# Performance work log

Measured on AMD Instinct MI355X. Metric: run time of the kernel, lower is better.

Reference implementation:

```python
import jax, jax.numpy as jnp
import numpy as np

HIDDEN = 1024
D_INNER = 2048      # expand * hidden
STATE = 16          # state_dim n
DT_RANK = 64        # ceil(hidden/16)
D_CONV = 4
B, S = 2, 2048
EPS = 1e-5


def setup_inputs() -> dict:
    key = jax.random.key(0)
    ks = jax.random.split(key, 10)
    sc = lambda fan_in: 1.0 / np.sqrt(fan_in)
    x = jax.random.normal(ks[0], (B, S, HIDDEN), dtype=jnp.float32)
    norm_w = jnp.ones((HIDDEN,), dtype=jnp.float32)
    in_proj_w = jax.random.uniform(ks[1], (2 * D_INNER, HIDDEN), minval=-sc(HIDDEN), maxval=sc(HIDDEN), dtype=jnp.float32)
    conv_w = jax.random.uniform(ks[2], (D_INNER, 1, D_CONV), minval=-sc(D_CONV), maxval=sc(D_CONV), dtype=jnp.float32)
    conv_b = jax.random.uniform(ks[3], (D_INNER,), minval=-sc(D_CONV), maxval=sc(D_CONV), dtype=jnp.float32)
    x_proj_w = jax.random.uniform(ks[4], (DT_RANK + 2 * STATE, D_INNER), minval=-sc(D_INNER), maxval=sc(D_INNER), dtype=jnp.float32)
    dt_proj_w = jax.random.uniform(ks[5], (D_INNER, DT_RANK), minval=-sc(DT_RANK), maxval=sc(DT_RANK), dtype=jnp.float32)
    dt_proj_b = jax.random.uniform(ks[6], (D_INNER,), minval=-sc(DT_RANK), maxval=sc(DT_RANK), dtype=jnp.float32)
    A_log = jnp.log(jnp.broadcast_to(jnp.arange(1, STATE + 1, dtype=jnp.float32), (D_INNER, STATE)))
    D = jnp.ones((D_INNER,), dtype=jnp.float32)
    out_proj_w = jax.random.uniform(ks[7], (HIDDEN, D_INNER), minval=-sc(D_INNER), maxval=sc(D_INNER), dtype=jnp.float32)
    return {"x": x, "norm_w": norm_w, "in_proj_w": in_proj_w, "conv_w": conv_w,
            "conv_b": conv_b, "x_proj_w": x_proj_w, "dt_proj_w": dt_proj_w,
            "dt_proj_b": dt_proj_b, "A_log": A_log, "D": D, "out_proj_w": out_proj_w}


def _selective_scan(u, delta, A, Bm, Cm, D):
    # u, delta: [b,s,d]; A: [d,n]; Bm, Cm: [b,s,n]; D: [d]
    deltaA = jnp.exp(jnp.einsum('bsd,dn->bsdn', delta, A))          # [b,s,d,n]
    deltaB_u = jnp.einsum('bsd,bsn,bsd->bsdn', delta, Bm, u)        # [b,s,d,n]

    def step(h, inp):
        dA_t, dBu_t, C_t = inp                                       # [b,d,n],[b,d,n],[b,n]
        h = dA_t * h + dBu_t
        y = jnp.einsum('bdn,bn->bd', h, C_t)
        return h, y

    h0 = jnp.zeros((u.shape[0], u.shape[2], A.shape[1]), dtype=u.dtype)
    _, ys = jax.lax.scan(step, h0,
                         (deltaA.transpose(1, 0, 2, 3),
                          deltaB_u.transpose(1, 0, 2, 3),
                          Cm.transpose(1, 0, 2)))
    y = ys.transpose(1, 0, 2)                                        # [b,s,d]
    return y + u * D


def reference(x, norm_w, in_proj_w, conv_w, conv_b, x_proj_w, dt_proj_w,
              dt_proj_b, A_log, D, out_proj_w):
    # RMSNorm
    xn = x * jax.lax.rsqrt(jnp.mean(x * x, axis=-1, keepdims=True) + EPS) * norm_w

    # in_proj -> split
    x_and_res = xn @ in_proj_w.T                                     # [b,s,2*d_inner]
    xi, res = jnp.split(x_and_res, 2, axis=-1)

    # causal depthwise conv1d (left-pad d_conv-1, truncate to s)
    xc = jax.lax.conv_general_dilated(
        xi.transpose(0, 2, 1), conv_w,
        window_strides=(1,), padding=[(D_CONV - 1, 0)],
        dimension_numbers=('NCH', 'OIH', 'NCH'),
        feature_group_count=D_INNER) + conv_b[None, :, None]
    xc = jax.nn.silu(xc.transpose(0, 2, 1))                          # [b,s,d_inner]

    # ssm
    A = -jnp.exp(A_log)
    x_dbl = xc @ x_proj_w.T                                          # [b,s,dt_rank+2n]
    dt, Bm, Cm = jnp.split(x_dbl, [DT_RANK, DT_RANK + STATE], axis=-1)
    delta = jax.nn.softplus(dt @ dt_proj_w.T + dt_proj_b)            # [b,s,d_inner]
    y = _selective_scan(xc, delta, A, Bm, Cm, D)

    y = y * jax.nn.silu(res)
    out = y @ out_proj_w.T
    return out + x
```

## Files before the change

kernel.cpp:

```cpp
#include <hip/hip_runtime.h>
#include <math.h>

#define HIDDEN   1024
#define D_INNER  2048
#define NSTATE   16
#define DT_RANK  64
#define BATCH    2
#define SEQ      2048
#define T_TOK    (BATCH * SEQ)
#define XDBL     (DT_RANK + 2 * NSTATE)
#define NCH      64
#define CHL      (SEQ / NCH)
#define BDN      (BATCH * D_INNER * NSTATE)

typedef float f32x4   __attribute__((ext_vector_type(4)));
typedef short bf16x8  __attribute__((ext_vector_type(8)));
typedef short short4v __attribute__((ext_vector_type(4)));

#define AS1 __attribute__((address_space(1)))
#define AS3 __attribute__((address_space(3)))
#define GLOAD(src, dst) __builtin_amdgcn_global_load_lds( \
    (const AS1 unsigned int*)(src), (AS3 unsigned int*)(dst), 16, 0, 0)

__device__ __forceinline__ float silu_f(float x) { return x / (1.0f + __expf(-x)); }
__device__ __forceinline__ float softplus_f(float x) {
    return fmaxf(x, 0.0f) + log1pf(__expf(-fabsf(x)));
}
__device__ __forceinline__ unsigned short f2bf(float x) {
    unsigned int u = __float_as_uint(x);
    u += 0x7fffu + ((u >> 16) & 1u);
    return (unsigned short)(u >> 16);
}
__device__ __forceinline__ float bf2f(unsigned short h) {
    return __uint_as_float(((unsigned int)h) << 16);
}

template<int SEGS>
__global__ __launch_bounds__(256) void wpack_kernel(
        const float* __restrict__ w, unsigned short* __restrict__ wp, int K) {
    int i = blockIdx.x * 256 + threadIdx.x;
    int kq = K >> 2;
    int row = i / kq;
    int c = (i - row * kq) << 2;
    float4 v = *(const float4*)(w + (size_t)row * K + c);
    short4v hi, lo;
    hi.x = f2bf(v.x); hi.y = f2bf(v.y); hi.z = f2bf(v.z); hi.w = f2bf(v.w);
    lo.x = f2bf(v.x - bf2f(hi.x)); lo.y = f2bf(v.y - bf2f(hi.y));
    lo.z = f2bf(v.z - bf2f(hi.z)); lo.w = f2bf(v.w - bf2f(hi.w));
    size_t b0 = (size_t)row * (SEGS * K) + c;
    *(short4v*)(wp + b0) = hi;
    if (SEGS == 2) *(short4v*)(wp + b0 + K) = lo;
}

__global__ __launch_bounds__(256) void rmsnorm_pack_kernel(
        const float* __restrict__ x, const float* __restrict__ w,
        unsigned short* __restrict__ xn_p) {
    int row = blockIdx.x;
    float4 v = ((const float4*)(x + (size_t)row * HIDDEN))[threadIdx.x];
    float ss = v.x*v.x + v.y*v.y + v.z*v.z + v.w*v.w;
    #pragma unroll
    for (int off = 32; off; off >>= 1) ss += __shfl_down(ss, off);
    __shared__ float wsum[4];
    if ((threadIdx.x & 63) == 0) wsum[threadIdx.x >> 6] = ss;
    __syncthreads();
    float scale = rsqrtf((wsum[0] + wsum[1] + wsum[2] + wsum[3]) / (float)HIDDEN + 1e-5f);
    float4 wv = ((const float4*)w)[threadIdx.x];
    float o0 = v.x * scale * wv.x, o1 = v.y * scale * wv.y;
    float o2 = v.z * scale * wv.z, o3 = v.w * scale * wv.w;
    short4v hi, lo;
    hi.x = f2bf(o0); hi.y = f2bf(o1); hi.z = f2bf(o2); hi.w = f2bf(o3);
    lo.x = f2bf(o0 - bf2f(hi.x)); lo.y = f2bf(o1 - bf2f(hi.y));
    lo.z = f2bf(o2 - bf2f(hi.z)); lo.w = f2bf(o3 - bf2f(hi.w));
    size_t b0 = (size_t)row * (2 * HIDDEN) + threadIdx.x * 4;
    *(short4v*)&xn_p[b0]          = hi;
    *(short4v*)&xn_p[b0 + HIDDEN] = lo;
}

__global__ __launch_bounds__(256, 2) void mgemm_in_kernel(
        const unsigned short* __restrict__ Ap,
        const unsigned short* __restrict__ Wp,
        float* __restrict__ C0, float* __restrict__ C1) {
    __shared__ short Ah[128 * 64];
    __shared__ short Al[128 * 64];
    __shared__ short Bh[256 * 64];
    const int t = threadIdx.x;
    const int w = t >> 6, l = t & 63;
    const int m0 = blockIdx.y * 128, n0 = blockIdx.x * 256;
    const int lrow = l & 15;
    f32x4 acc[8][4];
    #pragma unroll
    for (int m = 0; m < 8; ++m)
        #pragma unroll
        for (int n = 0; n < 4; ++n) {
            acc[m][n].x = 0.f; acc[m][n].y = 0.f; acc[m][n].z = 0.f; acc[m][n].w = 0.f;
        }
    const int srow8 = l >> 3;
    const int sc8   = (l & 7) ^ srow8;
    const unsigned short* ga = Ap + (size_t)(m0 + w * 32 + srow8) * 2048 + sc8 * 8;
    const unsigned short* gb = Wp + (size_t)(n0 + w * 64 + srow8) * 1024 + sc8 * 8;
    for (int k0 = 0; k0 < 1024; k0 += 64) {
        __syncthreads();
        #pragma unroll
        for (int q = 0; q < 4; ++q) {
            const int ar = (w * 32 + q * 8) * 128;
            GLOAD(ga + k0 + (size_t)q * 8 * 2048,        (char*)Ah + ar);
            GLOAD(ga + 1024 + k0 + (size_t)q * 8 * 2048, (char*)Al + ar);
        }
        #pragma unroll
        for (int q = 0; q < 8; ++q)
            GLOAD(gb + k0 + (size_t)q * 8 * 1024, (char*)Bh + (w * 64 + q * 8) * 128);
        __syncthreads();
        #pragma unroll
        for (int kk = 0; kk < 2; ++kk) {
            const int slot = ((kk * 4 + (l >> 4)) ^ (l & 7)) * 8;
            bf16x8 bh[4];
            #pragma unroll
            for (int n = 0; n < 4; ++n)
                bh[n] = *(const bf16x8*)&Bh[(w * 64 + n * 16 + lrow) * 64 + slot];
            #pragma unroll
            for (int m = 0; m < 8; ++m) {
                bf16x8 ah = *(const bf16x8*)&Ah[(m * 16 + lrow) * 64 + slot];
                bf16x8 al = *(const bf16x8*)&Al[(m * 16 + lrow) * 64 + slot];
                #pragma unroll
                for (int n = 0; n < 4; ++n) {
                    acc[m][n] = __builtin_amdgcn_mfma_f32_16x16x32_bf16(
                        ah, bh[n], acc[m][n], 0, 0, 0);
                    acc[m][n] = __builtin_amdgcn_mfma_f32_16x16x32_bf16(
                        al, bh[n], acc[m][n], 0, 0, 0);
                }
            }
        }
    }
    float* dst = (n0 < D_INNER) ? C0 : C1;
    const int cbase = (n0 < D_INNER) ? n0 : n0 - D_INNER;
    #pragma unroll
    for (int m = 0; m < 8; ++m) {
        #pragma unroll
        for (int n = 0; n < 4; ++n) {
            #pragma unroll
            for (int j = 0; j < 4; ++j) {
                int row = m0 + m * 16 + (l >> 4) * 4 + j;
                int col = cbase + w * 64 + n * 16 + (l & 15);
                dst[(size_t)row * D_INNER + col] = acc[m][n][j];
            }
        }
    }
}

template<int TERMS, int EPI>
__global__ __launch_bounds__(256) void mgemm_kernel(
        const unsigned short* __restrict__ Ap, const unsigned short* __restrict__ Wp,
        int Klog, int klen, int brows, float* __restrict__ C0, float* __restrict__ C1,
        int splitN, int ldout, size_t partStride, const float* __restrict__ bias) {
    constexpr int NT = (TERMS == 3) ? 4 : 3;
    __shared__ short lds[NT * 128 * 64];
    short* Ah = lds;
    short* Al = lds + 128 * 64;
    short* Bh = lds + 2 * 128 * 64;
    short* Bl = lds + 3 * 128 * 64;
    const int t = threadIdx.x;
    const int w = t >> 6, l = t & 63;
    const int m0 = blockIdx.y * 128, n0 = blockIdx.x * 128;
    const int kbeg = blockIdx.z * klen;
    const int wr = (w >> 1) * 64, wc = (w & 1) * 64;
    const int lrow = l & 15;
    f32x4 acc[4][4];
    #pragma unroll
    for (int m = 0; m < 4; ++m)
        #pragma unroll
        for (int n = 0; n < 4; ++n) {
            acc[m][n].x = 0.f; acc[m][n].y = 0.f; acc[m][n].z = 0.f; acc[m][n].w = 0.f;
        }
    const int Asr = 2 * Klog;
    const int Wsr = (TERMS == 3) ? 2 * Klog : Klog;
    const int srow = w * 32 + (l >> 3);
    const int sc8  = (l & 7) ^ ((l >> 3) & 7);
    const int brow = min(n0 + srow, brows - 1);
    const unsigned short* ga = Ap + (size_t)(m0 + srow) * Asr + sc8 * 8;
    const unsigned short* gb = Wp + (size_t)brow * Wsr + sc8 * 8;
    for (int k0 = kbeg; k0 < kbeg + klen; k0 += 64) {
        __syncthreads();
        #pragma unroll
        for (int q = 0; q < 4; ++q) {
            const int doff = (w * 32 + q * 8) * 128;
            GLOAD(ga + k0 + (size_t)q * 8 * Asr,        (char*)Ah + doff);
            GLOAD(ga + Klog + k0 + (size_t)q * 8 * Asr, (char*)Al + doff);
            GLOAD(gb + k0 + (size_t)q * 8 * Wsr,        (char*)Bh + doff);
            if (TERMS == 3)
                GLOAD(gb + Klog + k0 + (size_t)q * 8 * Wsr, (char*)Bl + doff);
        }
        __syncthreads();
        #pragma unroll
        for (int kk = 0; kk < 2; ++kk) {
            const int slot = ((kk * 4 + (l >> 4)) ^ (l & 7)) * 8;
            bf16x8 ah[4], al[4], bh[4], bl[4];
            #pragma unroll
            for (int m = 0; m < 4; ++m) {
                ah[m] = *(const bf16x8*)&Ah[(wr + m * 16 + lrow) * 64 + slot];
                al[m] = *(const bf16x8*)&Al[(wr + m * 16 + lrow) * 64 + slot];
            }
            #pragma unroll
            for (int n = 0; n < 4; ++n) {
                bh[n] = *(const bf16x8*)&Bh[(wc + n * 16 + lrow) * 64 + slot];
                if (TERMS == 3)
                    bl[n] = *(const bf16x8*)&Bl[(wc + n * 16 + lrow) * 64 + slot];
            }
            #pragma unroll
            for (int m = 0; m < 4; ++m)
                #pragma unroll
                for (int n = 0; n < 4; ++n) {
                    acc[m][n] = __builtin_amdgcn_mfma_f32_16x16x32_bf16(
                        ah[m], bh[n], acc[m][n], 0, 0, 0);
                    acc[m][n] = __builtin_amdgcn_mfma_f32_16x16x32_bf16(
                        al[m], bh[n], acc[m][n], 0, 0, 0);
                    if (TERMS == 3)
                        acc[m][n] = __builtin_amdgcn_mfma_f32_16x16x32_bf16(
                            ah[m], bl[n], acc[m][n], 0, 0, 0);
                }
        }
    }
    float* dst = (EPI == 2) ? (C0 + blockIdx.z * partStride) : C0;
    #pragma unroll
    for (int m = 0; m < 4; ++m) {
        #pragma unroll
        for (int n = 0; n < 4; ++n) {
            #pragma unroll
            for (int j = 0; j < 4; ++j) {
                int row = m0 + wr + m * 16 + (l >> 4) * 4 + j;
                int col = n0 + wc + n * 16 + (l & 15);
                float v = acc[m][n][j];
                if (EPI == 2) {
                    dst[(size_t)row * ldout + col] = v;
                } else {
                    C0[(size_t)row * ldout + col] = softplus_f(v + bias[col]);
                }
            }
        }
    }
}

__global__ __launch_bounds__(256) void reduce2_kernel(
        const float* __restrict__ parts, size_t partStride,
        const float* __restrict__ x, float* __restrict__ out) {
    size_t i = (size_t)blockIdx.x * 256 + threadIdx.x;
    float4 a = ((const float4*)(parts))[i];
    float4 b = ((const float4*)(parts + partStride))[i];
    float4 xv = ((const float4*)x)[i];
    float4 o;
    o.x = a.x + b.x + xv.x;
    o.y = a.y + b.y + xv.y;
    o.z = a.z + b.z + xv.z;
    o.w = a.w + b.w + xv.w;
    ((float4*)out)[i] = o;
}

__global__ __launch_bounds__(256) void reduceX_kernel(
        const float* __restrict__ parts, float* __restrict__ xdbl,
        unsigned short* __restrict__ dtp) {
    int i = blockIdx.x * 256 + threadIdx.x;
    int row = i / 24;
    int c = (i - row * 24) * 4;
    float4 s = make_float4(0.f, 0.f, 0.f, 0.f);
    #pragma unroll
    for (int z = 0; z < 8; ++z) {
        float4 a = *(const float4*)(parts + (size_t)z * 524288 + (size_t)row * 128 + c);
        s.x += a.x; s.y += a.y; s.z += a.z; s.w += a.w;
    }
    *(float4*)(xdbl + (size_t)row * XDBL + c) = s;
    if (c < DT_RANK) {
        short4v hi, lo;
        hi.x = f2bf(s.x); hi.y = f2bf(s.y); hi.z = f2bf(s.z); hi.w = f2bf(s.w);
        lo.x = f2bf(s.x - bf2f(hi.x)); lo.y = f2bf(s.y - bf2f(hi.y));
        lo.z = f2bf(s.z - bf2f(hi.z)); lo.w = f2bf(s.w - bf2f(hi.w));
        size_t b0 = (size_t)row * 128 + c;
        *(short4v*)(dtp + b0)      = hi;
        *(short4v*)(dtp + b0 + 64) = lo;
    }
}

__global__ __launch_bounds__(256) void conv_silu_kernel(
        const float* __restrict__ xi, const float* __restrict__ w,
        const float* __restrict__ b, unsigned short* __restrict__ xc_p) {
    size_t i = (size_t)blockIdx.x * 256 + threadIdx.x;
    int d = (int)(i & (D_INNER - 1));
    int tt = (int)(i >> 11);
    int s = tt & (SEQ - 1);
    float4 wv = ((const float4*)w)[d];
    float acc = b[d];
    if (s >= 3) acc += wv.x * xi[i - 3 * D_INNER];
    if (s >= 2) acc += wv.y * xi[i - 2 * D_INNER];
    if (s >= 1) acc += wv.z * xi[i - 1 * D_INNER];
    acc += wv.w * xi[i];
    float o = silu_f(acc);
    unsigned short hi = f2bf(o);
    unsigned short lo = f2bf(o - bf2f(hi));
    size_t o2 = (size_t)tt * (2 * D_INNER) + d;
    xc_p[o2]           = hi;
    xc_p[o2 + D_INNER] = lo;
}


__global__ __launch_bounds__(256) void scanA_kernel(
        const unsigned short* __restrict__ xcp, const float* __restrict__ delta,
        const float* __restrict__ xdbl, const float* __restrict__ A_log,
        float* __restrict__ hpart, float* __restrict__ Pp) {
    const int bid = blockIdx.x;
    const int b    = bid >> 9;
    const int c    = (bid >> 3) & 63;
    const int dblk = bid & 7;
    const int d    = (dblk << 8) + threadIdx.x;
    float adn[NSTATE];
    #pragma unroll
    for (int k = 0; k < 4; ++k) {
        float4 a = *(const float4*)(A_log + d * NSTATE + k * 4);
        adn[k*4+0] = -__expf(a.x); adn[k*4+1] = -__expf(a.y);
        adn[k*4+2] = -__expf(a.z); adn[k*4+3] = -__expf(a.w);
    }
    float h[NSTATE], P[NSTATE];
    #pragma unroll
    for (int n = 0; n < NSTATE; ++n) { h[n] = 0.f; P[n] = 1.f; }
    const int rowbase = b * SEQ + c * CHL;
    #pragma unroll 4
    for (int r = 0; r < CHL; ++r) {
        const int row = rowbase + r;
        const float* brow = xdbl + (size_t)row * XDBL + DT_RANK;
        size_t o2 = (size_t)row * (2 * D_INNER) + d;
        float dl = delta[(size_t)row * D_INNER + d];
        float u  = bf2f(xcp[o2]) + bf2f(xcp[o2 + D_INNER]);
        float du = dl * u;
        #pragma unroll
        for (int n = 0; n < NSTATE; ++n) {
            float dA = __expf(dl * adn[n]);
            h[n] = fmaf(dA, h[n], du * brow[n]);
            P[n] *= dA;
        }
    }
    size_t base = (size_t)c * BDN + (size_t)(b * D_INNER + d) * NSTATE;
    #pragma unroll
    for (int k = 0; k < 4; ++k) {
        *(float4*)(hpart + base + k * 4) = make_float4(h[k*4], h[k*4+1], h[k*4+2], h[k*4+3]);
        *(float4*)(Pp    + base + k * 4) = make_float4(P[k*4], P[k*4+1], P[k*4+2], P[k*4+3]);
    }
}

__global__ __launch_bounds__(256) void scanB_kernel(
        const float* __restrict__ hpart, const float* __restrict__ Pp,
        float* __restrict__ hstart) {
    int idx = blockIdx.x * 256 + threadIdx.x;
    float h = 0.f;
    for (int c = 0; c < NCH; ++c) {
        hstart[(size_t)c * BDN + idx] = h;
        h = fmaf(Pp[(size_t)c * BDN + idx], h, hpart[(size_t)c * BDN + idx]);
    }
}

__global__ __launch_bounds__(256) void scanC_kernel(
        const unsigned short* xcp, const float* __restrict__ delta,
        const float* __restrict__ xdbl, const float* __restrict__ A_log,
        const float* __restrict__ Dp, const float* __restrict__ hstart,
        const float* __restrict__ res, unsigned short* y_p) {
    const int bid = blockIdx.x;
    const int b    = bid >> 9;
    const int c    = (bid >> 3) & 63;
    const int dblk = bid & 7;
    const int d    = (dblk << 8) + threadIdx.x;
    float adn[NSTATE];
    #pragma unroll
    for (int k = 0; k < 4; ++k) {
        float4 a = *(const float4*)(A_log + d * NSTATE + k * 4);
        adn[k*4+0] = -__expf(a.x); adn[k*4+1] = -__expf(a.y);
        adn[k*4+2] = -__expf(a.z); adn[k*4+3] = -__expf(a.w);
    }
    const float Dd = Dp[d];
    float h[NSTATE];
    size_t base = (size_t)c * BDN + (size_t)(b * D_INNER + d) * NSTATE;
    #pragma unroll
    for (int k = 0; k < 4; ++k) {
        float4 hv = *(const float4*)(hstart + base + k * 4);
        h[k*4] = hv.x; h[k*4+1] = hv.y; h[k*4+2] = hv.z; h[k*4+3] = hv.w;
    }
    const int rowbase = b * SEQ + c * CHL;
    #pragma unroll 4
    for (int r = 0; r < CHL; ++r) {
        const int row = rowbase + r;
        const float* brow = xdbl + (size_t)row * XDBL + DT_RANK;
        const float* crow = brow + NSTATE;
        size_t o2 = (size_t)row * (2 * D_INNER) + d;
        float dl = delta[(size_t)row * D_INNER + d];
        float u  = bf2f(xcp[o2]) + bf2f(xcp[o2 + D_INNER]);
        float du = dl * u;
        float ys[4];
        ys[0] = u * Dd; ys[1] = 0.f; ys[2] = 0.f; ys[3] = 0.f;
        #pragma unroll
        for (int n = 0; n < NSTATE; ++n) {
            float dA = __expf(dl * adn[n]);
            h[n] = fmaf(dA, h[n], du * brow[n]);
            ys[n & 3] = fmaf(h[n], crow[n], ys[n & 3]);
        }
        float ysum = (ys[0] + ys[1]) + (ys[2] + ys[3]);
        float rv = res[(size_t)row * D_INNER + d];
        float gv = ysum * silu_f(rv);
        unsigned short hi = f2bf(gv);
        unsigned short lo = f2bf(gv - bf2f(hi));
        y_p[o2]           = hi;
        y_p[o2 + D_INNER] = lo;
    }
}

extern "C" void kernel_launch(void* const* d_in, const int* in_sizes, int n_in,
                              void* d_out, int out_size, void* d_ws, size_t ws_size,
                              hipStream_t stream) {
    const float* x         = (const float*)d_in[0];
    const float* norm_w    = (const float*)d_in[1];
    const float* in_proj_w = (const float*)d_in[2];
    const float* conv_w    = (const float*)d_in[3];
    const float* conv_b    = (const float*)d_in[4];
    const float* x_proj_w  = (const float*)d_in[5];
    const float* dt_proj_w = (const float*)d_in[6];
    const float* dt_proj_b = (const float*)d_in[7];
    const float* A_log     = (const float*)d_in[8];
    const float* Dp        = (const float*)d_in[9];
    const float* out_proj_w= (const float*)d_in[10];
    float* out = (float*)d_out;
    float* ws  = (float*)d_ws;

    const size_t M8 = (size_t)T_TOK * D_INNER;
    float* res   = ws;
    float* delta = res + M8;
    float* xdbl  = delta + M8;
    unsigned short* xn_p   = (unsigned short*)(xdbl + (size_t)T_TOK * XDBL);
    unsigned short* w_in_p = xn_p   + (size_t)4096 * 2048;
    unsigned short* w_out_p= w_in_p + (size_t)4096 * 1024;
    unsigned short* w_xp_p = w_out_p+ (size_t)1024 * 4096;
    unsigned short* w_dt_p = w_xp_p + (size_t)96 * 4096;
    unsigned short* xc_p   = w_dt_p + (size_t)2048 * 128;
    unsigned short* dtp_p  = xc_p   + (size_t)4096 * 4096;
    float* xi    = (float*)(dtp_p + (size_t)4096 * 128);
    float* hpart = xi;
    float* Pp    = xi + (size_t)BDN * NCH;
    float* hstart= (float*)xn_p;
    float* parts_x = delta;
    unsigned short* y_p = xc_p;
    float* parts = ws;
    const size_t partStride = (size_t)T_TOK * HIDDEN;

    wpack_kernel<1><<<4096, 256, 0, stream>>>(in_proj_w,  w_in_p,  HIDDEN);
    wpack_kernel<2><<<2048, 256, 0, stream>>>(out_proj_w, w_out_p, D_INNER);
    wpack_kernel<2><<<192,  256, 0, stream>>>(x_proj_w,   w_xp_p,  D_INNER);
    wpack_kernel<2><<<128,  256, 0, stream>>>(dt_proj_w,  w_dt_p,  DT_RANK);

    rmsnorm_pack_kernel<<<T_TOK, 256, 0, stream>>>(x, norm_w, xn_p);

    {
        dim3 g(4096 / 256, T_TOK / 128, 1);
        mgemm_in_kernel<<<g, 256, 0, stream>>>(xn_p, w_in_p, xi, res);
    }

    conv_silu_kernel<<<(int)(M8 / 256), 256, 0, stream>>>(xi, conv_w, conv_b, xc_p);

    {
        dim3 g(1, T_TOK / 128, 8);
        mgemm_kernel<3, 2><<<g, 256, 0, stream>>>(xc_p, w_xp_p, D_INNER, D_INNER / 8,
                                                  96, parts_x, nullptr, 0, 128, 524288, nullptr);
    }
    reduceX_kernel<<<T_TOK * 24 / 256, 256, 0, stream>>>(parts_x, xdbl, dtp_p);

    {
        dim3 g(D_INNER / 128, T_TOK / 128, 1);
        mgemm_kernel<3, 3><<<g, 256, 0, stream>>>(dtp_p, w_dt_p, DT_RANK, DT_RANK,
                                                  D_INNER, delta, nullptr, 0, D_INNER, 0, dt_proj_b);
    }

    scanA_kernel<<<BATCH * NCH * 8, 256, 0, stream>>>(xc_p, delta, xdbl, A_log, hpart, Pp);
    scanB_kernel<<<BDN / 256, 256, 0, stream>>>(hpart, Pp, hstart);
    scanC_kernel<<<BATCH * NCH * 8, 256, 0, stream>>>(xc_p, delta, xdbl, A_log, Dp, hstart, res, y_p);

    {
        dim3 g(HIDDEN / 128, T_TOK / 128, 2);
        mgemm_kernel<3, 2><<<g, 256, 0, stream>>>(y_p, w_out_p, D_INNER, D_INNER / 2,
                                                  HIDDEN, parts, nullptr, 0, HIDDEN, partStride, nullptr);
    }
    reduce2_kernel<<<(int)(partStride / 4 / 256), 256, 0, stream>>>(parts, partStride, x, out);
}
```

Before: 312.7 us.

## Add 8-wave double-buffered 256x256 split-bf16 GEMM for in/out projections

Replaces the in_proj GEMM and the out_proj GEMM with a new 512-thread kernel using a 256x256 tile. It double-buffers LDS stages and interleaves global-to-LDS loads with MFMA phases, using barriers and s_setprio. Operands are packed as concatenated hi/lo (and hi/hi/lo) K segments, so each term pair runs as a single longer K loop. The out projection uses a 4-way K split with a 4-way reduce, and the workspace layout is rearranged. This adds barrier overhead and more packed data in exchange for better MFMA utilisation and load overlap.

```diff
diff --git a/kernel.cpp b/kernel.cpp
--- a/kernel.cpp
+++ b/kernel.cpp
@@ -35,7 +35,7 @@
     return __uint_as_float(((unsigned int)h) << 16);
 }
 
-template<int SEGS>
+template<int MODE>
 __global__ __launch_bounds__(256) void wpack_kernel(
         const float* __restrict__ w, unsigned short* __restrict__ wp, int K) {
     int i = blockIdx.x * 256 + threadIdx.x;
@@ -47,9 +47,18 @@
     hi.x = f2bf(v.x); hi.y = f2bf(v.y); hi.z = f2bf(v.z); hi.w = f2bf(v.w);
     lo.x = f2bf(v.x - bf2f(hi.x)); lo.y = f2bf(v.y - bf2f(hi.y));
     lo.z = f2bf(v.z - bf2f(hi.z)); lo.w = f2bf(v.w - bf2f(hi.w));
-    size_t b0 = (size_t)row * (SEGS * K) + c;
-    *(short4v*)(wp + b0) = hi;
-    if (SEGS == 2) *(short4v*)(wp + b0 + K) = lo;
+    size_t b0 = (size_t)row * ((MODE == 2 ? 3 : 2) * K) + c;
+    if (MODE == 0) {
+        *(short4v*)(wp + b0)     = hi;
+        *(short4v*)(wp + b0 + K) = lo;
+    } else if (MODE == 1) {
+        *(short4v*)(wp + b0)     = hi;
+        *(short4v*)(wp + b0 + K) = hi;
+    } else {
+        *(short4v*)(wp + b0)         = hi;
+        *(short4v*)(wp + b0 + K)     = lo;
+        *(short4v*)(wp + b0 + 2 * K) = hi;
+    }
 }
 
 __global__ __launch_bounds__(256) void rmsnorm_pack_kernel(
@@ -76,17 +85,21 @@
     *(short4v*)&xn_p[b0 + HIDDEN] = lo;
 }
 
-__global__ __launch_bounds__(256, 2) void mgemm_in_kernel(
-        const unsigned short* __restrict__ Ap,
-        const unsigned short* __restrict__ Wp,
-        float* __restrict__ C0, float* __restrict__ C1) {
-    __shared__ short Ah[128 * 64];
-    __shared__ short Al[128 * 64];
-    __shared__ short Bh[256 * 64];
+template<int EPI>
+__global__ __launch_bounds__(512, 2) void mgemm8_kernel(
+        const unsigned short* __restrict__ Ap, const unsigned short* __restrict__ Wp,
+        int Kp, int klen, float* __restrict__ C0, float* __restrict__ C1,
+        int ldout, size_t partStride) {
+    __shared__ short lds8[65536];
     const int t = threadIdx.x;
     const int w = t >> 6, l = t & 63;
-    const int m0 = blockIdx.y * 128, n0 = blockIdx.x * 256;
+    const int wm = w >> 2, wn = w & 3;
+    const int m0 = blockIdx.y * 256, n0 = blockIdx.x * 256;
+    const int kbeg = blockIdx.z * klen;
+    const int NT = klen >> 6;
     const int lrow = l & 15;
+    const int sl0 = (((l >> 4)    ) ^ (l & 7)) * 8;
+    const int sl1 = (((l >> 4) + 4) ^ (l & 7)) * 8;
     f32x4 acc[8][4];
     #pragma unroll
     for (int m = 0; m < 8; ++m)
@@ -96,52 +109,112 @@
         }
     const int srow8 = l >> 3;
     const int sc8   = (l & 7) ^ srow8;
-    const unsigned short* ga = Ap + (size_t)(m0 + w * 32 + srow8) * 2048 + sc8 * 8;
-    const unsigned short* gb = Wp + (size_t)(n0 + w * 64 + srow8) * 1024 + sc8 * 8;
-    for (int k0 = 0; k0 < 1024; k0 += 64) {
-        __syncthreads();
-        #pragma unroll
-        for (int q = 0; q < 4; ++q) {
-            const int ar = (w * 32 + q * 8) * 128;
-            GLOAD(ga + k0 + (size_t)q * 8 * 2048,        (char*)Ah + ar);
-            GLOAD(ga + 1024 + k0 + (size_t)q * 8 * 2048, (char*)Al + ar);
-        }
-        #pragma unroll
-        for (int q = 0; q < 8; ++q)
-            GLOAD(gb + k0 + (size_t)q * 8 * 1024, (char*)Bh + (w * 64 + q * 8) * 128);
-        __syncthreads();
-        #pragma unroll
-        for (int kk = 0; kk < 2; ++kk) {
-            const int slot = ((kk * 4 + (l >> 4)) ^ (l & 7)) * 8;
-            bf16x8 bh[4];
+    const unsigned short* gA = Ap + (size_t)(m0 + w * 8 + srow8) * Kp + kbeg + sc8 * 8;
+    const unsigned short* gB = Wp + (size_t)(n0 + w * 8 + srow8) * Kp + kbeg + sc8 * 8;
+    auto stageA = [&](int c, int koff) {
+        #pragma unroll
+        for (int hq = 0; hq < 4; ++hq)
+            GLOAD(gA + (size_t)(hq * 64) * Kp + koff,
+                  (char*)lds8 + ((c * 2 + (hq >> 1)) * 16384)
+                              + ((hq & 1) * 64 + w * 8) * 128);
+    };
+    auto stageB = [&](int c, int koff) {
+        #pragma unroll
+        for (int hq = 0; hq < 4; ++hq)
+            GLOAD(gB + (size_t)(hq * 64) * Kp + koff,
+                  (char*)lds8 + 65536 + ((c * 2 + (hq >> 1)) * 16384)
+                              + ((hq & 1) * 64 + w * 8) * 128);
+    };
+    stageA(0, 0);
+    stageB(0, 0);
+    asm volatile("s_waitcnt vmcnt(0)" ::: "memory");
+    __builtin_amdgcn_s_barrier();
+    for (int tt = 0; tt < NT; ++tt) {
+        const int c = tt & 1;
+        const int knext = (tt + 1) * 64;
+        const bool more = (tt + 1 < NT);
+        const short* Ab = lds8 + (c * 2 + wm) * 8192;
+        const short* Bb = lds8 + 32768 + (c * 2 + (wn >> 1)) * 8192;
+        const int br0 = (wn & 1) * 64;
+        bf16x8 bh[4], af[4];
+        #pragma unroll
+        for (int n = 0; n < 4; ++n)
+            bh[n] = *(const bf16x8*)&Bb[(br0 + n * 16 + lrow) * 64 + sl0];
+        #pragma unroll
+        for (int m = 0; m < 4; ++m)
+            af[m] = *(const bf16x8*)&Ab[(m * 16 + lrow) * 64 + sl0];
+        if (more) stageA(c ^ 1, knext);
+        __builtin_amdgcn_s_barrier();
+        asm volatile("s_waitcnt lgkmcnt(0)" ::: "memory");
+        __builtin_amdgcn_s_setprio(1);
+        #pragma unroll
+        for (int m = 0; m < 4; ++m)
             #pragma unroll
             for (int n = 0; n < 4; ++n)
-                bh[n] = *(const bf16x8*)&Bh[(w * 64 + n * 16 + lrow) * 64 + slot];
-            #pragma unroll
-            for (int m = 0; m < 8; ++m) {
-                bf16x8 ah = *(const bf16x8*)&Ah[(m * 16 + lrow) * 64 + slot];
-                bf16x8 al = *(const bf16x8*)&Al[(m * 16 + lrow) * 64 + slot];
-                #pragma unroll
-                for (int n = 0; n < 4; ++n) {
-                    acc[m][n] = __builtin_amdgcn_mfma_f32_16x16x32_bf16(
-                        ah, bh[n], acc[m][n], 0, 0, 0);
-                    acc[m][n] = __builtin_amdgcn_mfma_f32_16x16x32_bf16(
-                        al, bh[n], acc[m][n], 0, 0, 0);
-                }
-            }
-        }
-    }
-    float* dst = (n0 < D_INNER) ? C0 : C1;
-    const int cbase = (n0 < D_INNER) ? n0 : n0 - D_INNER;
+                acc[m][n] = __builtin_amdgcn_mfma_f32_16x16x32_bf16(
+                    af[m], bh[n], acc[m][n], 0, 0, 0);
+        __builtin_amdgcn_s_setprio(0);
+        __builtin_amdgcn_s_barrier();
+        #pragma unroll
+        for (int m = 0; m < 4; ++m)
+            af[m] = *(const bf16x8*)&Ab[((m + 4) * 16 + lrow) * 64 + sl0];
+        if (more) stageB(c ^ 1, knext);
+        __builtin_amdgcn_s_barrier();
+        asm volatile("s_waitcnt lgkmcnt(0)" ::: "memory");
+        __builtin_amdgcn_s_setprio(1);
+        #pragma unroll
+        for (int m = 0; m < 4; ++m)
+            #pragma unroll
+            for (int n = 0; n < 4; ++n)
+                acc[m + 4][n] = __builtin_amdgcn_mfma_f32_16x16x32_bf16(
+                    af[m], bh[n], acc[m + 4][n], 0, 0, 0);
+        __builtin_amdgcn_s_setprio(0);
+        __builtin_amdgcn_s_barrier();
+        #pragma unroll
+        for (int n = 0; n < 4; ++n)
+            bh[n] = *(const bf16x8*)&Bb[(br0 + n * 16 + lrow) * 64 + sl1];
+        #pragma unroll
+        for (int m = 0; m < 4; ++m)
+            af[m] = *(const bf16x8*)&Ab[(m * 16 + lrow) * 64 + sl1];
+        __builtin_amdgcn_s_barrier();
+        asm volatile("s_waitcnt lgkmcnt(0)" ::: "memory");
+        __builtin_amdgcn_s_setprio(1);
+        #pragma unroll
+        for (int m = 0; m < 4; ++m)
+            #pragma unroll
+            for (int n = 0; n < 4; ++n)
+                acc[m][n] = __builtin_amdgcn_mfma_f32_16x16x32_bf16(
+                    af[m], bh[n], acc[m][n], 0, 0, 0);
+        __builtin_amdgcn_s_setprio(0);
+        __builtin_amdgcn_s_barrier();
+        #pragma unroll
+        for (int m = 0; m < 4; ++m)
+            af[m] = *(const bf16x8*)&Ab[((m + 4) * 16 + lrow) * 64 + sl1];
+        __builtin_amdgcn_s_barrier();
+        asm volatile("s_waitcnt lgkmcnt(0)" ::: "memory");
+        __builtin_amdgcn_s_setprio(1);
+        #pragma unroll
+        for (int m = 0; m < 4; ++m)
+            #pragma unroll
+            for (int n = 0; n < 4; ++n)
+                acc[m + 4][n] = __builtin_amdgcn_mfma_f32_16x16x32_bf16(
+                    af[m], bh[n], acc[m + 4][n], 0, 0, 0);
+        __builtin_amdgcn_s_setprio(0);
+        asm volatile("s_waitcnt vmcnt(0)" ::: "memory");
+        __builtin_amdgcn_s_barrier();
+    }
+    float* dstp = (EPI == 2) ? (C0 + blockIdx.z * partStride)
+                             : ((n0 < D_INNER) ? C0 : C1);
+    const int cb = (EPI == 0 && n0 >= D_INNER) ? D_INNER : 0;
     #pragma unroll
     for (int m = 0; m < 8; ++m) {
         #pragma unroll
         for (int n = 0; n < 4; ++n) {
             #pragma unroll
             for (int j = 0; j < 4; ++j) {
-                int row = m0 + m * 16 + (l >> 4) * 4 + j;
-                int col = cbase + w * 64 + n * 16 + (l & 15);
-                dst[(size_t)row * D_INNER + col] = acc[m][n][j];
+                int row = m0 + wm * 128 + m * 16 + (l >> 4) * 4 + j;
+                int col = n0 + wn * 64 + n * 16 + (l & 15);
+                dstp[(size_t)row * ldout + (col - cb)] = acc[m][n][j];
             }
         }
     }
@@ -239,18 +312,20 @@
     }
 }
 
-__global__ __launch_bounds__(256) void reduce2_kernel(
+__global__ __launch_bounds__(256) void reduce4_kernel(
         const float* __restrict__ parts, size_t partStride,
         const float* __restrict__ x, float* __restrict__ out) {
     size_t i = (size_t)blockIdx.x * 256 + threadIdx.x;
     float4 a = ((const float4*)(parts))[i];
     float4 b = ((const float4*)(parts + partStride))[i];
+    float4 c = ((const float4*)(parts + 2 * partStride))[i];
+    float4 d = ((const float4*)(parts + 3 * partStride))[i];
     float4 xv = ((const float4*)x)[i];
     float4 o;
-    o.x = a.x + b.x + xv.x;
-    o.y = a.y + b.y + xv.y;
-    o.z = a.z + b.z + xv.z;
-    o.w = a.w + b.w + xv.w;
+    o.x = a.x + b.x + c.x + d.x + xv.x;
+    o.y = a.y + b.y + c.y + d.y + xv.y;
+    o.z = a.z + b.z + c.z + d.z + xv.z;
+    o.w = a.w + b.w + c.w + d.w + xv.w;
     ((float4*)out)[i] = o;
 }
 
@@ -355,10 +430,10 @@
 }
 
 __global__ __launch_bounds__(256) void scanC_kernel(
-        const unsigned short* xcp, const float* __restrict__ delta,
+        const unsigned short* __restrict__ xcp, const float* __restrict__ delta,
         const float* __restrict__ xdbl, const float* __restrict__ A_log,
         const float* __restrict__ Dp, const float* __restrict__ hstart,
-        const float* __restrict__ res, unsigned short* y_p) {
+        const float* __restrict__ res, unsigned short* __restrict__ y_p) {
     const int bid = blockIdx.x;
     const int b    = bid >> 9;
     const int c    = (bid >> 3) & 63;
@@ -402,8 +477,10 @@
         float gv = ysum * silu_f(rv);
         unsigned short hi = f2bf(gv);
         unsigned short lo = f2bf(gv - bf2f(hi));
-        y_p[o2]           = hi;
-        y_p[o2 + D_INNER] = lo;
+        size_t o6 = (size_t)row * (3 * D_INNER) + d;
+        y_p[o6]                = hi;
+        y_p[o6 + D_INNER]      = hi;
+        y_p[o6 + 2 * D_INNER]  = lo;
     }
 }
 
@@ -426,34 +503,42 @@
 
     const size_t M8 = (size_t)T_TOK * D_INNER;
     float* res   = ws;
-    float* delta = res + M8;
-    float* xdbl  = delta + M8;
-    unsigned short* xn_p   = (unsigned short*)(xdbl + (size_t)T_TOK * XDBL);
-    unsigned short* w_in_p = xn_p   + (size_t)4096 * 2048;
-    unsigned short* w_out_p= w_in_p + (size_t)4096 * 1024;
-    unsigned short* w_xp_p = w_out_p+ (size_t)1024 * 4096;
-    unsigned short* w_dt_p = w_xp_p + (size_t)96 * 4096;
-    unsigned short* xc_p   = w_dt_p + (size_t)2048 * 128;
-    unsigned short* dtp_p  = xc_p   + (size_t)4096 * 4096;
-    float* xi    = (float*)(dtp_p + (size_t)4096 * 128);
-    float* hpart = xi;
-    float* Pp    = xi + (size_t)BDN * NCH;
-    float* hstart= (float*)xn_p;
+    float* delta = ws + M8;
+    float* xdbl  = ws + 2 * M8;
+    size_t off = 2 * M8 + 393216;
+    unsigned short* xn_p   = (unsigned short*)(ws + off);
+    unsigned short* w_in_p = xn_p + (size_t)4096 * 2048;
+    float* xi = ws + off + 8388608;
+    unsigned short* y_p = xn_p;
+    size_t off2 = off + 16777216;
+    unsigned short* w_out_p = (unsigned short*)(ws + off2);
+    size_t off3 = off2 + 3145728;
+    unsigned short* w_xp_p = (unsigned short*)(ws + off3);
+    size_t off4 = off3 + 196608;
+    unsigned short* w_dt_p = (unsigned short*)(ws + off4);
+    size_t off5 = off4 + 131072;
+    unsigned short* xc_p = (unsigned short*)(ws + off5);
+    size_t off6 = off5 + 8388608;
+    unsigned short* dtp_p = (unsigned short*)(ws + off6);
+    size_t off7 = off6 + 262144;
+    float* hpart  = ws + off7;
+    float* Pp     = hpart + 4194304;
+    float* hstart = Pp + 4194304;
     float* parts_x = delta;
-    unsigned short* y_p = xc_p;
-    float* parts = ws;
+    float* parts   = ws + off5;
     const size_t partStride = (size_t)T_TOK * HIDDEN;
 
     wpack_kernel<1><<<4096, 256, 0, stream>>>(in_proj_w,  w_in_p,  HIDDEN);
     wpack_kernel<2><<<2048, 256, 0, stream>>>(out_proj_w, w_out_p, D_INNER);
-    wpack_kernel<2><<<192,  256, 0, stream>>>(x_proj_w,   w_xp_p,  D_INNER);
-    wpack_kernel<2><<<128,  256, 0, stream>>>(dt_proj_w,  w_dt_p,  DT_RANK);
+    wpack_kernel<0><<<192,  256, 0, stream>>>(x_proj_w,   w_xp_p,  D_INNER);
+    wpack_kernel<0><<<128,  256, 0, stream>>>(dt_proj_w,  w_dt_p,  DT_RANK);
 
     rmsnorm_pack_kernel<<<T_TOK, 256, 0, stream>>>(x, norm_w, xn_p);
 
     {
-        dim3 g(4096 / 256, T_TOK / 128, 1);
-        mgemm_in_kernel<<<g, 256, 0, stream>>>(xn_p, w_in_p, xi, res);
+        dim3 g(4096 / 256, T_TOK / 256, 1);
+        mgemm8_kernel<0><<<g, 512, 0, stream>>>(xn_p, w_in_p, 2 * HIDDEN, 2 * HIDDEN,
+                                                xi, res, D_INNER, 0);
     }
 
     conv_silu_kernel<<<(int)(M8 / 256), 256, 0, stream>>>(xi, conv_w, conv_b, xc_p);
@@ -476,9 +561,9 @@
     scanC_kernel<<<BATCH * NCH * 8, 256, 0, stream>>>(xc_p, delta, xdbl, A_log, Dp, hstart, res, y_p);
 
     {
-        dim3 g(HIDDEN / 128, T_TOK / 128, 2);
-        mgemm_kernel<3, 2><<<g, 256, 0, stream>>>(y_p, w_out_p, D_INNER, D_INNER / 2,
-                                                  HIDDEN, parts, nullptr, 0, HIDDEN, partStride, nullptr);
-    }
-    reduce2_kernel<<<(int)(partStride / 4 / 256), 256, 0, stream>>>(parts, partStride, x, out);
-}
+        dim3 g(HIDDEN / 256, T_TOK / 256, 4);
+        mgemm8_kernel<2><<<g, 512, 0, stream>>>(y_p, w_out_p, 3 * D_INNER, 6144 / 4,
+                                                parts, nullptr, HIDDEN, partStride);
+    }
+    reduce4_kernel<<<(int)(partStride / 4 / 256), 256, 0, stream>>>(parts, partStride, x, out);
+}
```

Result: no change. 318.6 us (+1.9%).
